# Kernel optimization log

Measured on AMD Instinct MI355X. Metric: run time of the kernel, lower is better.

The kernel has to match this reference:

```python
import jax, jax.numpy as jnp
import numpy as np
import math

B, C, H, W = 32, 384, 64, 64      # batch, backbone dim, feature-map HxW
E, NH = 256, 16                   # embed_dim, num_heads (grapsules per image)
HD = E // NH                      # head dim
RFF_HALF, HID = 32, 128           # RFF rows (out=64), GNN hidden


def setup_inputs() -> dict:
    key = jax.random.key(0)
    ks = jax.random.split(key, 10)
    rn = lambda k, s: (0.02 * jax.random.normal(k, s)).astype(jnp.float32)
    x = jax.random.normal(ks[0], (B, C, H, W), jnp.float32)
    qw = rn(ks[1], (E, C)); qb = jnp.zeros((E,), jnp.float32)
    kw = rn(ks[2], (E, C)); kb = jnp.zeros((E,), jnp.float32)
    vw = rn(ks[3], (E, C)); vb = jnp.zeros((E,), jnp.float32)
    # RFF B ~ N(0,1) * sigma * 2*pi, sigma=1.0
    B_rff = (jax.random.normal(ks[4], (RFF_HALF, 2)) * (2.0 * math.pi)).astype(jnp.float32)
    msg_w = rn(ks[5], (HID, E)); msg_b = jnp.zeros((HID,), jnp.float32)
    emb_w = rn(ks[6], (HID, 2 * RFF_HALF))
    lin1_w = rn(ks[7], (4 * HID, HID)); lin1_b = jnp.zeros((4 * HID,), jnp.float32)
    lin2_w = rn(ks[8], (E, 4 * HID)); lin2_b = jnp.zeros((E,), jnp.float32)
    layer_scale = jnp.full((1, E), 1e-6, jnp.float32)
    # fully-connected directed graph (no self loops) among the NH grapsules of each image
    pairs = np.array([(i, j) for i in range(NH) for j in range(NH) if i != j], dtype=np.int32)
    off = (np.arange(B, dtype=np.int32) * NH)[:, None]
    edge_src = jnp.asarray((pairs[:, 0][None, :] + off).reshape(-1))
    edge_dst = jnp.asarray((pairs[:, 1][None, :] + off).reshape(-1))
    return dict(x=x, qw=qw, qb=qb, kw=kw, kb=kb, vw=vw, vb=vb, B_rff=B_rff,
                msg_w=msg_w, msg_b=msg_b, emb_w=emb_w, lin1_w=lin1_w, lin1_b=lin1_b,
                lin2_w=lin2_w, lin2_b=lin2_b, layer_scale=layer_scale,
                edge_src=edge_src, edge_dst=edge_dst)


def _forward(x, qw, qb, kw, kb, vw, vb, B_rff, msg_w, msg_b, emb_w,
             lin1_w, lin1_b, lin2_w, lin2_b, layer_scale, edge_src, edge_dst):
    Bsz, Cc, Hh, Ww = x.shape
    N = Hh * Ww
    # --- ImageToGraphTransformer (attention pooling to grapsule nodes) ---
    xf = x.reshape(Bsz, Cc, N).transpose(0, 2, 1)            # [B,N,C]
    xm = xf.mean(axis=1)                                     # [B,C]
    q = (xm @ qw.T + qb).reshape(Bsz, NH, HD)                # [B,h,d]
    k = (xf @ kw.T + kb).reshape(Bsz, N, NH, HD)             # [B,N,h,d]
    v = xf @ vw.T + vb                                       # [B,N,E]
    logits = jnp.einsum('bhc,bnhc->bnh', q, k) / math.sqrt(HD)
    attn = jax.nn.softmax(logits, axis=1)                    # softmax over pixels
    xx, yy = jnp.meshgrid(jnp.arange(Hh, dtype=x.dtype), jnp.arange(Ww, dtype=x.dtype), indexing='ij')
    pos_grid = jnp.stack((xx.reshape(-1), yy.reshape(-1)), axis=-1)  # [N,2]
    values = jnp.einsum('bnh,bnc->bhc', attn, v).reshape(Bsz * NH, E)
    pos = jnp.einsum('bnh,nx->bhx', attn, pos_grid).reshape(Bsz * NH, 2)
    # --- RFF embedding of relative positions (edge_attr) ---
    rel = pos[edge_src] - pos[edge_dst]                      # [Eg,2]
    proj = rel @ B_rff.T                                     # [Eg,32]
    edge_attr = math.sqrt(2.0) * jnp.concatenate((jnp.sin(proj), jnp.cos(proj)), axis=-1)
    # --- Conv (MessagePassing) with ConditionalLinear 'strong', mean aggr ---
    m = (values[edge_src] @ msg_w.T + msg_b) * (edge_attr @ emb_w.T)   # [Eg,HID]
    agg = jax.ops.segment_sum(m, edge_dst, num_segments=Bsz * NH) / (NH - 1)
    # --- ConvBlockNeXt MLP + layer scale + identity skip (in==out) ---
    h = jax.nn.silu(agg @ lin1_w.T + lin1_b)
    o = h @ lin2_w.T + lin2_b
    return layer_scale * o + values


def reference(x, qw, qb, kw, kb, vw, vb, B_rff, msg_w, msg_b, emb_w,
              lin1_w, lin1_b, lin2_w, lin2_b, layer_scale, edge_src, edge_dst):
    return _forward(x, qw, qb, kw, kb, vw, vb, B_rff, msg_w, msg_b, emb_w,
                    lin1_w, lin1_b, lin2_w, lin2_b, layer_scale, edge_src, edge_dst)
```

## Files before the change

kernel.cpp:

```cpp
#include <hip/hip_runtime.h>
#include <math.h>


#define Bsz 32
#define Cc  384
#define Nn  4096
#define Ee  256
#define NHh 16
#define HDd 16
#define HIDh 128

__device__ __forceinline__ float waveSum(float v){
#pragma unroll
  for(int o=32;o;o>>=1) v += __shfl_down(v,(unsigned)o,64);
  return v;
}
__device__ __forceinline__ float waveMax(float v){
#pragma unroll
  for(int o=32;o;o>>=1) v = fmaxf(v, __shfl_down(v,(unsigned)o,64));
  return v;
}
__device__ __forceinline__ float blockSum(float v, float* sm){
  int lane = threadIdx.x & 63, w = threadIdx.x >> 6;
  int nw = blockDim.x >> 6;
  float r = waveSum(v);
  if(lane==0) sm[w] = r;
  __syncthreads();
  float s = 0.f;
  for(int i=0;i<nw;i++) s += sm[i];
  __syncthreads();
  return s;
}
__device__ __forceinline__ float blockMax(float v, float* sm){
  int lane = threadIdx.x & 63, w = threadIdx.x >> 6;
  int nw = blockDim.x >> 6;
  float r = waveMax(v);
  if(lane==0) sm[w] = r;
  __syncthreads();
  float s = -1e30f;
  for(int i=0;i<nw;i++) s = fmaxf(s, sm[i]);
  __syncthreads();
  return s;
}

__global__ __launch_bounds__(256) void k_mean(const float* __restrict__ x, float* __restrict__ xm){
  int bc = blockIdx.x, t = threadIdx.x;
  const float4* xr = (const float4*)(x + (size_t)bc*Nn);
  float s = 0.f;
#pragma unroll
  for(int i=0;i<4;i++){ float4 v = xr[t + 256*i]; s += (v.x+v.y) + (v.z+v.w); }
  __shared__ float sm[8];
  s = blockSum(s, sm);
  if(t==0) xm[bc] = s * (1.0f/4096.0f);
}

__global__ __launch_bounds__(384) void k_qk(const float* __restrict__ xm, const float* __restrict__ qw,
                                            const float* __restrict__ qb, const float* __restrict__ kw,
                                            float* __restrict__ qk_t){
  int b = blockIdx.x, t = threadIdx.x;
  __shared__ float xs[Cc];
  __shared__ float qs[Ee];
  if(t < 96) ((float4*)xs)[t] = ((const float4*)(xm + b*Cc))[t];
  __syncthreads();
  if(t < Ee){
    const float4* wr = (const float4*)(qw + (size_t)t*Cc);
    const float4* xv = (const float4*)xs;
    float a = qb[t];
#pragma unroll 4
    for(int c4=0;c4<96;c4++){ float4 w = wr[c4], xx = xv[c4]; a += w.x*xx.x + w.y*xx.y + w.z*xx.z + w.w*xx.w; }
    qs[t] = a;
  }
  __syncthreads();
  int c = t;
#pragma unroll
  for(int hq=0; hq<4; hq++){
    float r0, r1, r2, r3;
#pragma unroll
    for(int hh=0; hh<4; hh++){
      int h = hq*4 + hh;
      float a = 0.f;
#pragma unroll
      for(int d=0; d<16; d++) a += qs[h*16+d] * kw[(size_t)(h*16+d)*Cc + c];
      a *= 0.25f;
      if(hh==0) r0=a; else if(hh==1) r1=a; else if(hh==2) r2=a; else r3=a;
    }
    ((float4*)(qk_t + ((size_t)b*Cc + c)*16))[hq] = make_float4(r0,r1,r2,r3);
  }
}

__global__ __launch_bounds__(256) void k_logits(const float* __restrict__ x, const float* __restrict__ qk_t,
                                                float* __restrict__ lg){
  int b = blockIdx.y;
  int n = blockIdx.x*256 + threadIdx.x;
  float acc[16];
#pragma unroll
  for(int h=0;h<16;h++) acc[h] = 0.f;
  const float* xb = x + (size_t)b*Cc*Nn;
  const float4* qk = (const float4*)(qk_t + (size_t)b*Cc*16);
#pragma unroll 8
  for(int c=0;c<Cc;c++){
    float xv = xb[(size_t)c*Nn + n];
    float4 q0 = qk[c*4+0], q1 = qk[c*4+1], q2 = qk[c*4+2], q3 = qk[c*4+3];
    acc[0]  += xv*q0.x; acc[1]  += xv*q0.y; acc[2]  += xv*q0.z; acc[3]  += xv*q0.w;
    acc[4]  += xv*q1.x; acc[5]  += xv*q1.y; acc[6]  += xv*q1.z; acc[7]  += xv*q1.w;
    acc[8]  += xv*q2.x; acc[9]  += xv*q2.y; acc[10] += xv*q2.z; acc[11] += xv*q2.w;
    acc[12] += xv*q3.x; acc[13] += xv*q3.y; acc[14] += xv*q3.z; acc[15] += xv*q3.w;
  }
#pragma unroll
  for(int h=0;h<16;h++) lg[((size_t)(b*16+h))*Nn + n] = acc[h];
}

__global__ __launch_bounds__(256) void k_softmax(float* __restrict__ lg, float* __restrict__ pos){
  int node = blockIdx.x, t = threadIdx.x;
  __shared__ float sm[8];
  float4* gv = (float4*)(lg + (size_t)node*Nn);
  float4 vv[4];
  float m = -1e30f;
#pragma unroll
  for(int i=0;i<4;i++){
    vv[i] = gv[t + 256*i];
    m = fmaxf(m, fmaxf(fmaxf(vv[i].x, vv[i].y), fmaxf(vv[i].z, vv[i].w)));
  }
  m = blockMax(m, sm);
  float s = 0.f, px = 0.f, py = 0.f;
  float4 ev[4];
#pragma unroll
  for(int i=0;i<4;i++){
    int n0 = 4*(t + 256*i);
    float e0 = __expf(vv[i].x - m), e1 = __expf(vv[i].y - m);
    float e2 = __expf(vv[i].z - m), e3 = __expf(vv[i].w - m);
    float row = (float)(n0 >> 6);
    float c0  = (float)(n0 & 63);
    float es  = (e0+e1)+(e2+e3);
    s  += es;
    px += es * row;
    py += e0*c0 + e1*(c0+1.f) + e2*(c0+2.f) + e3*(c0+3.f);
    ev[i] = make_float4(e0,e1,e2,e3);
  }
  s  = blockSum(s,  sm);
  px = blockSum(px, sm);
  py = blockSum(py, sm);
  float inv = 1.0f / s;
#pragma unroll
  for(int i=0;i<4;i++)
    gv[t + 256*i] = make_float4(ev[i].x*inv, ev[i].y*inv, ev[i].z*inv, ev[i].w*inv);
  if(t==0){ pos[node*2] = px*inv; pos[node*2+1] = py*inv; }
}

#define XROW 36
__global__ __launch_bounds__(256) void k_xa(const float* __restrict__ x, const float* __restrict__ attn,
                                            float* __restrict__ part){
  __shared__ float xl[Cc*XROW];
  __shared__ float al[NHh*XROW];
  int b = blockIdx.y, ns = blockIdx.x, t = threadIdx.x;
  int th = t & 3, tc = t >> 2;
  float acc[4][6];
#pragma unroll
  for(int k=0;k<4;k++)
#pragma unroll
    for(int m=0;m<6;m++) acc[k][m] = 0.f;

  float4 xr[12];
  float4 ar = make_float4(0,0,0,0);
  int ah = t >> 3, aj = t & 7;

  auto LOAD = [&](int ch){
    int n0 = ns*256 + ch*32;
    if(t < 128)
      ar = *(const float4*)(attn + ((size_t)(b*16+ah))*Nn + n0 + aj*4);
#pragma unroll
    for(int i=0;i<12;i++){
      int f = t + 256*i;
      int c = f >> 3, j4 = f & 7;
      xr[i] = *(const float4*)(x + ((size_t)(b*Cc+c))*Nn + n0 + j4*4);
    }
  };

  LOAD(0);
  for(int ch=0; ch<8; ch++){
    if(t < 128) *(float4*)(al + ah*XROW + aj*4) = ar;
#pragma unroll
    for(int i=0;i<12;i++){
      int f = t + 256*i;
      int c = f >> 3, j4 = f & 7;
      *(float4*)(xl + c*XROW + j4*4) = xr[i];
    }
    __syncthreads();
    if(ch < 7) LOAD(ch+1);
#pragma unroll
    for(int j4=0;j4<8;j4++){
      float4 a4[4], x4[6];
#pragma unroll
      for(int k=0;k<4;k++) a4[k] = *(const float4*)(al + (th+4*k)*XROW + j4*4);
#pragma unroll
      for(int m=0;m<6;m++) x4[m] = *(const float4*)(xl + (tc+64*m)*XROW + j4*4);
#pragma unroll
      for(int k=0;k<4;k++)
#pragma unroll
        for(int m=0;m<6;m++)
          acc[k][m] += a4[k].x*x4[m].x + a4[k].y*x4[m].y + a4[k].z*x4[m].z + a4[k].w*x4[m].w;
    }
    __syncthreads();
  }
#pragma unroll
  for(int k=0;k<4;k++)
#pragma unroll
    for(int m=0;m<6;m++)
      part[(size_t)ns*(Bsz*NHh*Cc) + (size_t)(b*16 + th + 4*k)*Cc + (tc + 64*m)] = acc[k][m];
}

__global__ __launch_bounds__(256) void k_values(const float* __restrict__ part, const float* __restrict__ vw,
                                                const float* __restrict__ vb, const float* __restrict__ msg_w,
                                                const float* __restrict__ msg_b,
                                                float* __restrict__ values, float* __restrict__ msgv){
  int node = blockIdx.x, t = threadIdx.x;
  __shared__ float xa[Cc];
  __shared__ float vs[Ee];
  if(t < 96){
    float4 s = make_float4(0,0,0,0);
#pragma unroll
    for(int p=0;p<16;p++){
      float4 v = *(const float4*)(part + (size_t)p*(Bsz*NHh*Cc) + (size_t)node*Cc + t*4);
      s.x += v.x; s.y += v.y; s.z += v.z; s.w += v.w;
    }
    *(float4*)(xa + t*4) = s;
  }
  __syncthreads();
  {
    const float4* wr = (const float4*)(vw + (size_t)t*Cc);
    const float4* xv = (const float4*)xa;
    float a = vb[t];
#pragma unroll 4
    for(int c4=0;c4<96;c4++){ float4 w = wr[c4], xx = xv[c4]; a += w.x*xx.x + w.y*xx.y + w.z*xx.z + w.w*xx.w; }
    values[(size_t)node*Ee + t] = a;
    vs[t] = a;
  }
  __syncthreads();
  if(t < HIDh){
    const float4* mr = (const float4*)(msg_w + (size_t)t*Ee);
    const float4* vv = (const float4*)vs;
    float a = msg_b[t];
#pragma unroll 4
    for(int e4=0;e4<64;e4++){ float4 w = mr[e4], xx = vv[e4]; a += w.x*xx.x + w.y*xx.y + w.z*xx.z + w.w*xx.w; }
    msgv[(size_t)node*HIDh + t] = a;
  }
}

__global__ __launch_bounds__(128) void k_agg(const float* __restrict__ pos, const float* __restrict__ msgv,
                                             const float* __restrict__ brff, const float* __restrict__ emb_w,
                                             float* __restrict__ agg){
  int node = blockIdx.x, t = threadIdx.x;
  int b = node >> 4, jj = node & 15;
  __shared__ float ps[32];
  __shared__ float bf[64];
  __shared__ float mv[16*HIDh];
  __shared__ float ea[64];
  if(t < 32) ps[t] = pos[b*32 + t];
  if(t < 64) bf[t] = brff[t];
#pragma unroll
  for(int i=0;i<4;i++){ int f = t + 128*i; ((float4*)mv)[f] = ((const float4*)(msgv + (size_t)b*16*HIDh))[f]; }
  float4 er[16];
#pragma unroll
  for(int i=0;i<16;i++) er[i] = ((const float4*)(emb_w + (size_t)t*64))[i];
  __syncthreads();
  float pxj = ps[jj*2], pyj = ps[jj*2+1];
  float acc = 0.f;
  for(int i=0;i<16;i++){
    if(i == jj) continue;
    float rx = ps[i*2]   - pxj;
    float ry = ps[i*2+1] - pyj;
    __syncthreads();
    if(t < 32){
      float pr = rx*bf[t*2] + ry*bf[t*2+1];
      ea[t]    = 1.41421356f * __sinf(pr);
      ea[t+32] = 1.41421356f * __cosf(pr);
    }
    __syncthreads();
    float psi = 0.f;
    const float4* eav = (const float4*)ea;
#pragma unroll
    for(int k=0;k<16;k++){ float4 e4 = eav[k]; psi += e4.x*er[k].x + e4.y*er[k].y + e4.z*er[k].z + e4.w*er[k].w; }
    acc += mv[i*HIDh + t] * psi;
  }
  agg[(size_t)node*HIDh + t] = acc * (1.0f/15.0f);
}

__global__ __launch_bounds__(256) void k_mlp(const float* __restrict__ agg, const float* __restrict__ l1w,
                                             const float* __restrict__ l1b, const float* __restrict__ l2w,
                                             const float* __restrict__ l2b, const float* __restrict__ ls,
                                             const float* __restrict__ values, float* __restrict__ out){
  int node = blockIdx.x, t = threadIdx.x;
  __shared__ float ag[HIDh];
  __shared__ float h1[512];
  if(t < 32) ((float4*)ag)[t] = ((const float4*)(agg + (size_t)node*HIDh))[t];
  __syncthreads();
#pragma unroll
  for(int r=0;r<2;r++){
    int u = t + r*256;
    const float4* wr = (const float4*)(l1w + (size_t)u*HIDh);
    const float4* av = (const float4*)ag;
    float a = l1b[u];
#pragma unroll 4
    for(int k=0;k<32;k++){ float4 w = wr[k], xx = av[k]; a += w.x*xx.x + w.y*xx.y + w.z*xx.z + w.w*xx.w; }
    h1[u] = a / (1.0f + __expf(-a));
  }
  __syncthreads();
  {
    const float4* wr = (const float4*)(l2w + (size_t)t*512);
    const float4* hv = (const float4*)h1;
    float o = l2b[t];
#pragma unroll 4
    for(int k=0;k<128;k++){ float4 w = wr[k], xx = hv[k]; o += w.x*xx.x + w.y*xx.y + w.z*xx.z + w.w*xx.w; }
    size_t oi = (size_t)node*Ee + t;
    out[oi] = ls[t]*o + values[oi];
  }
}

extern "C" void kernel_launch(void* const* d_in, const int* in_sizes, int n_in,
                              void* d_out, int out_size, void* d_ws, size_t ws_size,
                              hipStream_t stream) {
  const float* x    = (const float*)d_in[0];
  const float* qw   = (const float*)d_in[1];
  const float* qb   = (const float*)d_in[2];
  const float* kw   = (const float*)d_in[3];
  const float* vw   = (const float*)d_in[5];
  const float* vb   = (const float*)d_in[6];
  const float* brff = (const float*)d_in[7];
  const float* msgw = (const float*)d_in[8];
  const float* msgb = (const float*)d_in[9];
  const float* embw = (const float*)d_in[10];
  const float* l1w  = (const float*)d_in[11];
  const float* l1b  = (const float*)d_in[12];
  const float* l2w  = (const float*)d_in[13];
  const float* l2b  = (const float*)d_in[14];
  const float* lsc  = (const float*)d_in[15];

  float* W      = (float*)d_ws;
  float* xm     = W;
  float* qkt    = xm  + 12288;
  float* lg     = qkt + 196608;
  float* pos    = lg  + 2097152;
  float* part   = pos + 1024;
  float* values = part + 3145728;
  float* msgv   = values + 131072;
  float* agg    = msgv + 65536;
  float* out    = (float*)d_out;

  k_mean   <<<Bsz*Cc, 256, 0, stream>>>(x, xm);
  k_qk     <<<Bsz, 384, 0, stream>>>(xm, qw, qb, kw, qkt);
  k_logits <<<dim3(16, Bsz), 256, 0, stream>>>(x, qkt, lg);
  k_softmax<<<Bsz*NHh, 256, 0, stream>>>(lg, pos);
  k_xa     <<<dim3(16, Bsz), 256, 0, stream>>>(x, lg, part);
  k_values <<<Bsz*NHh, 256, 0, stream>>>(part, vw, vb, msgw, msgb, values, msgv);
  k_agg    <<<Bsz*NHh, 128, 0, stream>>>(pos, msgv, brff, embw, agg);
  k_mlp    <<<Bsz*NHh, 256, 0, stream>>>(agg, l1w, l1b, l2w, l2b, lsc, values, out);
}
```

Measured before the change: 580.4 us.

## Fuse softmax into logits and attention-pooling kernels via online-softmax partials

Removes the standalone softmax kernel. k_logits now stages the per-batch qk matrix in shared memory and emits per-tile (max, sum, pos-x, pos-y) partial statistics. k_xa merges those partials, rescales them, and applies exp/normalize while loading raw logits, which drops a full read/write pass over the logits buffer and one launch. In exchange it adds shared-memory pressure and extra exp work per k_xa block, since each of the 16 tiles recomputes the merge.

```diff
diff --git a/kernel.cpp b/kernel.cpp
--- a/kernel.cpp
+++ b/kernel.cpp
@@ -7,7 +7,6 @@
 #define Nn  4096
 #define Ee  256
 #define NHh 16
-#define HDd 16
 #define HIDh 128
 
 __device__ __forceinline__ float waveSum(float v){
@@ -15,9 +14,14 @@
   for(int o=32;o;o>>=1) v += __shfl_down(v,(unsigned)o,64);
   return v;
 }
-__device__ __forceinline__ float waveMax(float v){
-#pragma unroll
-  for(int o=32;o;o>>=1) v = fmaxf(v, __shfl_down(v,(unsigned)o,64));
+__device__ __forceinline__ float waveMaxAll(float v){
+#pragma unroll
+  for(int o=1;o<64;o<<=1) v = fmaxf(v, __shfl_xor(v,(unsigned)o,64));
+  return v;
+}
+__device__ __forceinline__ float waveSumAll(float v){
+#pragma unroll
+  for(int o=1;o<64;o<<=1) v += __shfl_xor(v,(unsigned)o,64);
   return v;
 }
 __device__ __forceinline__ float blockSum(float v, float* sm){
@@ -28,17 +32,6 @@
   __syncthreads();
   float s = 0.f;
   for(int i=0;i<nw;i++) s += sm[i];
-  __syncthreads();
-  return s;
-}
-__device__ __forceinline__ float blockMax(float v, float* sm){
-  int lane = threadIdx.x & 63, w = threadIdx.x >> 6;
-  int nw = blockDim.x >> 6;
-  float r = waveMax(v);
-  if(lane==0) sm[w] = r;
-  __syncthreads();
-  float s = -1e30f;
-  for(int i=0;i<nw;i++) s = fmaxf(s, sm[i]);
   __syncthreads();
   return s;
 }
@@ -89,18 +82,26 @@
 }
 
 __global__ __launch_bounds__(256) void k_logits(const float* __restrict__ x, const float* __restrict__ qk_t,
-                                                float* __restrict__ lg){
-  int b = blockIdx.y;
-  int n = blockIdx.x*256 + threadIdx.x;
+                                                float* __restrict__ lg, float* __restrict__ spart){
+  __shared__ float qks[Cc*16];
+  int b = blockIdx.y, ns = blockIdx.x, t = threadIdx.x;
+  int n = ns*256 + t;
+  {
+    const float4* src = (const float4*)(qk_t + (size_t)b*Cc*16);
+    float4* dst = (float4*)qks;
+#pragma unroll
+    for(int i=0;i<6;i++) dst[t + 256*i] = src[t + 256*i];
+  }
+  __syncthreads();
   float acc[16];
 #pragma unroll
   for(int h=0;h<16;h++) acc[h] = 0.f;
-  const float* xb = x + (size_t)b*Cc*Nn;
-  const float4* qk = (const float4*)(qk_t + (size_t)b*Cc*16);
+  const float* xb = x + (size_t)b*Cc*Nn + n;
 #pragma unroll 8
   for(int c=0;c<Cc;c++){
-    float xv = xb[(size_t)c*Nn + n];
-    float4 q0 = qk[c*4+0], q1 = qk[c*4+1], q2 = qk[c*4+2], q3 = qk[c*4+3];
+    float xv = xb[(size_t)c*Nn];
+    const float4* qv = (const float4*)(qks + c*16);
+    float4 q0 = qv[0], q1 = qv[1], q2 = qv[2], q3 = qv[3];
     acc[0]  += xv*q0.x; acc[1]  += xv*q0.y; acc[2]  += xv*q0.z; acc[3]  += xv*q0.w;
     acc[4]  += xv*q1.x; acc[5]  += xv*q1.y; acc[6]  += xv*q1.z; acc[7]  += xv*q1.w;
     acc[8]  += xv*q2.x; acc[9]  += xv*q2.y; acc[10] += xv*q2.z; acc[11] += xv*q2.w;
@@ -108,52 +109,66 @@
   }
 #pragma unroll
   for(int h=0;h<16;h++) lg[((size_t)(b*16+h))*Nn + n] = acc[h];
-}
-
-__global__ __launch_bounds__(256) void k_softmax(float* __restrict__ lg, float* __restrict__ pos){
-  int node = blockIdx.x, t = threadIdx.x;
-  __shared__ float sm[8];
-  float4* gv = (float4*)(lg + (size_t)node*Nn);
-  float4 vv[4];
-  float m = -1e30f;
-#pragma unroll
-  for(int i=0;i<4;i++){
-    vv[i] = gv[t + 256*i];
-    m = fmaxf(m, fmaxf(fmaxf(vv[i].x, vv[i].y), fmaxf(vv[i].z, vv[i].w)));
-  }
-  m = blockMax(m, sm);
-  float s = 0.f, px = 0.f, py = 0.f;
-  float4 ev[4];
-#pragma unroll
-  for(int i=0;i<4;i++){
-    int n0 = 4*(t + 256*i);
-    float e0 = __expf(vv[i].x - m), e1 = __expf(vv[i].y - m);
-    float e2 = __expf(vv[i].z - m), e3 = __expf(vv[i].w - m);
-    float row = (float)(n0 >> 6);
-    float c0  = (float)(n0 & 63);
-    float es  = (e0+e1)+(e2+e3);
-    s  += es;
-    px += es * row;
-    py += e0*c0 + e1*(c0+1.f) + e2*(c0+2.f) + e3*(c0+3.f);
-    ev[i] = make_float4(e0,e1,e2,e3);
-  }
-  s  = blockSum(s,  sm);
-  px = blockSum(px, sm);
-  py = blockSum(py, sm);
-  float inv = 1.0f / s;
-#pragma unroll
-  for(int i=0;i<4;i++)
-    gv[t + 256*i] = make_float4(ev[i].x*inv, ev[i].y*inv, ev[i].z*inv, ev[i].w*inv);
-  if(t==0){ pos[node*2] = px*inv; pos[node*2+1] = py*inv; }
+
+  __syncthreads();
+  float* sl = qks;
+#pragma unroll
+  for(int h=0;h<16;h++) sl[h*256 + t] = acc[h];
+  __syncthreads();
+  int w = t >> 6, lane = t & 63;
+#pragma unroll
+  for(int hh=0; hh<4; hh++){
+    int h = w*4 + hh;
+    float v0 = sl[h*256 + lane], v1 = sl[h*256 + 64 + lane];
+    float v2 = sl[h*256 + 128 + lane], v3 = sl[h*256 + 192 + lane];
+    float m = waveMaxAll(fmaxf(fmaxf(v0,v1), fmaxf(v2,v3)));
+    float e0 = __expf(v0-m), e1 = __expf(v1-m), e2 = __expf(v2-m), e3 = __expf(v3-m);
+    float row0 = (float)(ns*4);
+    float col  = (float)lane;
+    float s  = (e0+e1)+(e2+e3);
+    float px = e0*row0 + e1*(row0+1.f) + e2*(row0+2.f) + e3*(row0+3.f);
+    float py = s * col;
+    float s_t  = waveSumAll(s);
+    float px_t = waveSumAll(px);
+    float py_t = waveSumAll(py);
+    if(lane==0)
+      *(float4*)(spart + ((size_t)(b*16+h)*16 + ns)*4) = make_float4(m, s_t, px_t, py_t);
+  }
 }
 
 #define XROW 36
-__global__ __launch_bounds__(256) void k_xa(const float* __restrict__ x, const float* __restrict__ attn,
+__global__ __launch_bounds__(256) void k_xa(const float* __restrict__ x, const float* __restrict__ lg,
+                                            const float* __restrict__ spart, float* __restrict__ pos,
                                             float* __restrict__ part){
   __shared__ float xl[Cc*XROW];
   __shared__ float al[NHh*XROW];
+  __shared__ float ss[32];
   int b = blockIdx.y, ns = blockIdx.x, t = threadIdx.x;
   int th = t & 3, tc = t >> 2;
+  if(t < 64){
+    int h = t >> 2, qq = t & 3;
+    const float4* sp = (const float4*)spart + (size_t)(b*16+h)*16 + qq*4;
+    float4 p0 = sp[0], p1 = sp[1], p2 = sp[2], p3 = sp[3];
+    float m = fmaxf(fmaxf(p0.x,p1.x), fmaxf(p2.x,p3.x));
+    m = fmaxf(m, __shfl_xor(m, 1u, 64));
+    m = fmaxf(m, __shfl_xor(m, 2u, 64));
+    float w0 = __expf(p0.x-m), w1 = __expf(p1.x-m), w2 = __expf(p2.x-m), w3 = __expf(p3.x-m);
+    float s  = p0.y*w0 + p1.y*w1 + p2.y*w2 + p3.y*w3;
+    float px = p0.z*w0 + p1.z*w1 + p2.z*w2 + p3.z*w3;
+    float py = p0.w*w0 + p1.w*w1 + p2.w*w2 + p3.w*w3;
+    s  += __shfl_xor(s, 1u, 64);  s  += __shfl_xor(s, 2u, 64);
+    px += __shfl_xor(px,1u, 64);  px += __shfl_xor(px,2u, 64);
+    py += __shfl_xor(py,1u, 64);  py += __shfl_xor(py,2u, 64);
+    if(qq==0){
+      float inv = 1.0f/s;
+      ss[h*2] = m; ss[h*2+1] = inv;
+      if(ns==0){ pos[(b*16+h)*2] = px*inv; pos[(b*16+h)*2+1] = py*inv; }
+    }
+  }
+  __syncthreads();
+  int ah = t >> 3, aj = t & 7;
+  float mA = 0.f, iA = 0.f;
+  if(t < 128){ mA = ss[ah*2]; iA = ss[ah*2+1]; }
   float acc[4][6];
 #pragma unroll
   for(int k=0;k<4;k++)
@@ -162,12 +177,11 @@
 
   float4 xr[12];
   float4 ar = make_float4(0,0,0,0);
-  int ah = t >> 3, aj = t & 7;
 
   auto LOAD = [&](int ch){
     int n0 = ns*256 + ch*32;
     if(t < 128)
-      ar = *(const float4*)(attn + ((size_t)(b*16+ah))*Nn + n0 + aj*4);
+      ar = *(const float4*)(lg + ((size_t)(b*16+ah))*Nn + n0 + aj*4);
 #pragma unroll
     for(int i=0;i<12;i++){
       int f = t + 256*i;
@@ -178,7 +192,14 @@
 
   LOAD(0);
   for(int ch=0; ch<8; ch++){
-    if(t < 128) *(float4*)(al + ah*XROW + aj*4) = ar;
+    if(t < 128){
+      float4 e;
+      e.x = __expf(ar.x - mA)*iA;
+      e.y = __expf(ar.y - mA)*iA;
+      e.z = __expf(ar.z - mA)*iA;
+      e.w = __expf(ar.w - mA)*iA;
+      *(float4*)(al + ah*XROW + aj*4) = e;
+    }
 #pragma unroll
     for(int i=0;i<12;i++){
       int f = t + 256*i;
@@ -340,18 +361,18 @@
   float* qkt    = xm  + 12288;
   float* lg     = qkt + 196608;
   float* pos    = lg  + 2097152;
-  float* part   = pos + 1024;
+  float* spart  = pos + 1024;
+  float* part   = spart + 32768;
   float* values = part + 3145728;
   float* msgv   = values + 131072;
   float* agg    = msgv + 65536;
   float* out    = (float*)d_out;
 
-  k_mean   <<<Bsz*Cc, 256, 0, stream>>>(x, xm);
-  k_qk     <<<Bsz, 384, 0, stream>>>(xm, qw, qb, kw, qkt);
-  k_logits <<<dim3(16, Bsz), 256, 0, stream>>>(x, qkt, lg);
-  k_softmax<<<Bsz*NHh, 256, 0, stream>>>(lg, pos);
-  k_xa     <<<dim3(16, Bsz), 256, 0, stream>>>(x, lg, part);
-  k_values <<<Bsz*NHh, 256, 0, stream>>>(part, vw, vb, msgw, msgb, values, msgv);
-  k_agg    <<<Bsz*NHh, 128, 0, stream>>>(pos, msgv, brff, embw, agg);
-  k_mlp    <<<Bsz*NHh, 256, 0, stream>>>(agg, l1w, l1b, l2w, l2b, lsc, values, out);
-}
+  k_mean  <<<Bsz*Cc, 256, 0, stream>>>(x, xm);
+  k_qk    <<<Bsz, 384, 0, stream>>>(xm, qw, qb, kw, qkt);
+  k_logits<<<dim3(16, Bsz), 256, 0, stream>>>(x, qkt, lg, spart);
+  k_xa    <<<dim3(16, Bsz), 256, 0, stream>>>(x, lg, spart, pos, part);
+  k_values<<<Bsz*NHh, 256, 0, stream>>>(part, vw, vb, msgw, msgb, values, msgv);
+  k_agg   <<<Bsz*NHh, 128, 0, stream>>>(pos, msgv, brff, embw, agg);
+  k_mlp   <<<Bsz*NHh, 256, 0, stream>>>(agg, l1w, l1b, l2w, l2b, lsc, values, out);
+}
```

New measurement: 564.9 us. -2.7%, faster.
